# Kernel tuning notes

Hardware: AMD Instinct MI355X
Metric: run time of the kernel (lower is better)

The kernel has to match this reference:

```python
import jax, jax.numpy as jnp
import numpy as np

ROPE_BASE = 1000.0  # note: module uses base=1000, not the usual 10000


def _rope(x):
    # x: [B, L, H, d]; rotates the full head dim (x_pass is empty since d == hid_head)
    d = x.shape[-1]
    L = x.shape[1]
    theta = 1.0 / (ROPE_BASE ** (jnp.arange(0, d, 2, dtype=jnp.float32) / d))  # [d/2]
    idx = jnp.arange(L, dtype=jnp.float32)[:, None] * theta[None, :]            # [L, d/2]
    idx2 = jnp.concatenate([idx, idx], axis=-1)                                 # [L, d]
    cos = jnp.cos(idx2)[:, None, :]  # [L, 1, d] -> broadcasts over B, H
    sin = jnp.sin(idx2)[:, None, :]
    half = d // 2
    neg_half = jnp.concatenate([-x[..., half:], x[..., :half]], axis=-1)
    return x * cos + neg_half * sin


def setup_inputs() -> dict:
    key = jax.random.key(0)
    ks = jax.random.split(key, 8)
    B, Lq, Lc, F = 4, 1024, 2047, 2048
    s = 0.02
    return {
        "kv": jax.random.normal(ks[0], (B, 1, F), jnp.float32),
        "q": jax.random.normal(ks[1], (B, Lq, F), jnp.float32),
        "kv_cache": jax.random.normal(ks[2], (B, Lc, F, 2), jnp.float32),
        "Wq": jax.random.normal(ks[3], (F, F), jnp.float32) * s,
        "Wk": jax.random.normal(ks[4], (F, F), jnp.float32) * s,
        "Wv": jax.random.normal(ks[5], (F, F), jnp.float32) * s,
        "Wo": jax.random.normal(ks[6], (F, F), jnp.float32) * s,
        "mask": jnp.ones((B, 1, Lq, Lc + 1), jnp.int32),
        "num_heads": 16,
    }


def reference(kv, q, kv_cache, Wq, Wk, Wv, Wo, mask, num_heads):
    B = q.shape[0]
    F = Wq.shape[1]
    hd = F // num_heads

    query = q @ Wq                          # [B, Lq, F]
    key_new = kv[:, -1, :] @ Wk             # [B, F] (only last kv token is projected)
    val_new = kv[:, -1, :] @ Wv             # [B, F]

    key = jnp.concatenate([kv_cache[..., 0], key_new[:, None, :]], axis=1)    # [B, Lk, F]
    value = jnp.concatenate([kv_cache[..., 1], val_new[:, None, :]], axis=1)  # [B, Lk, F]
    kv_cache_out = jnp.stack([key, value], axis=-1)                            # [B, Lk, F, 2]

    query = query.reshape(B, -1, num_heads, hd)   # [B, Lq, H, d]
    key = key.reshape(B, -1, num_heads, hd)       # [B, Lk, H, d]
    value = value.reshape(B, -1, num_heads, hd)   # [B, Lk, H, d]

    query = _rope(query)
    key = _rope(key)

    aw = jnp.einsum('bqhd,bkhd->bhqk', query, key) / jnp.sqrt(jnp.float32(hd))
    aw = jnp.where(mask > 0, aw, -jnp.inf)  # mask [B,1,Lq,Lk] broadcasts over heads
    aw = jax.nn.softmax(aw, axis=-1)

    out = jnp.einsum('bhqk,bkhd->bqhd', aw, value).reshape(B, -1, F)
    logits = out @ Wo
    return logits, kv_cache_out
```

## Files before the change

### kernel.cpp

```cpp
#include <hip/hip_runtime.h>

#define B_  4
#define LQ  1024
#define LC  2047
#define LK  2048
#define F_  2048
#define H_  16
#define DH  128

typedef __attribute__((ext_vector_type(4))) float f32x4;
typedef __attribute__((ext_vector_type(8))) __bf16 bf16x8;
typedef __attribute__((ext_vector_type(8))) unsigned short u16x8;

#define GLD16(gp, lp)                                                          \
  __builtin_amdgcn_global_load_lds(                                            \
      (const __attribute__((address_space(1))) void*)(gp),                     \
      (__attribute__((address_space(3))) void*)(lp), 16, 0, 0)

__device__ __forceinline__ unsigned short f2bf(float f) {
  unsigned u = __float_as_uint(f);
  u += 0x7FFFu + ((u >> 16) & 1u);
  return (unsigned short)(u >> 16);
}
__device__ __forceinline__ unsigned short f2bf_trunc(float f) {
  return (unsigned short)(__float_as_uint(f) >> 16);
}
__device__ __forceinline__ float bf2f(unsigned short u) {
  return __uint_as_float((unsigned)u << 16);
}

__global__ void k_tables(float* __restrict__ cost, float* __restrict__ sint) {
  int pos = blockIdx.x, j = threadIdx.x;
  float theta = powf(1000.0f, -(float)j / 64.0f);
  float a = (float)pos * theta;
  cost[pos * 64 + j] = cosf(a);
  sint[pos * 64 + j] = sinf(a);
}

__global__ void k_gemv_part(const float* __restrict__ kv, const float* __restrict__ Wk,
                            const float* __restrict__ Wv, float* __restrict__ part) {
  __shared__ float kvs[4][256];
  int tid = threadIdx.x, z = blockIdx.z;
#pragma unroll
  for (int b = 0; b < 4; ++b) kvs[b][tid] = kv[b * F_ + z * 256 + tid];
  __syncthreads();
  const float* W = blockIdx.y ? Wv : Wk;
  int col = blockIdx.x * 256 + tid;
  float a0 = 0.f, a1 = 0.f, a2 = 0.f, a3 = 0.f;
  for (int k = 0; k < 256; ++k) {
    float w = W[(size_t)(z * 256 + k) * F_ + col];
    a0 = fmaf(kvs[0][k], w, a0);
    a1 = fmaf(kvs[1][k], w, a1);
    a2 = fmaf(kvs[2][k], w, a2);
    a3 = fmaf(kvs[3][k], w, a3);
  }
  float* o = part + (size_t)(blockIdx.y * 8 + z) * 8192;
  o[col] = a0; o[2048 + col] = a1; o[4096 + col] = a2; o[6144 + col] = a3;
}

__global__ void k_gemv_reduce(const float* __restrict__ part, float* __restrict__ knew,
                              float* __restrict__ vnew) {
  int t = blockIdx.x * 256 + threadIdx.x;
  int y = t >> 13, idx = t & 8191;
  float s = 0.f;
#pragma unroll
  for (int z = 0; z < 8; ++z) s += part[(size_t)(y * 8 + z) * 8192 + idx];
  (y ? vnew : knew)[idx] = s;
}

__global__ void k_prep_kv(const float* __restrict__ cache, const float* __restrict__ knew,
                          const float* __restrict__ vnew, const float* __restrict__ cost,
                          const float* __restrict__ sint, float* __restrict__ cache_out,
                          unsigned short* __restrict__ Kr, unsigned short* __restrict__ Vb) {
  int t = blockIdx.x * 256 + threadIdx.x;
  int j = t & 63, h = (t >> 6) & 15, pos = (t >> 10) & 2047, b = t >> 21;
  int f = h * DH + j;
  float k1, v1, k2, v2;
  if (pos < LC) {
    const float* p = cache + ((size_t)(b * LC + pos) * F_ + f) * 2;
    float2 x = *(const float2*)p;
    float2 y = *(const float2*)(p + 128);
    k1 = x.x; v1 = x.y; k2 = y.x; v2 = y.y;
  } else {
    k1 = knew[b * F_ + f];      v1 = vnew[b * F_ + f];
    k2 = knew[b * F_ + f + 64]; v2 = vnew[b * F_ + f + 64];
  }
  float* o = cache_out + ((size_t)(b * LK + pos) * F_ + f) * 2;
  *(float2*)o = make_float2(k1, v1);
  *(float2*)(o + 128) = make_float2(k2, v2);
  float c = cost[pos * 64 + j], s = sint[pos * 64 + j];
  size_t kb = ((size_t)(b * H_ + h) * LK + pos) * DH + j;
  Kr[kb]      = f2bf(k1 * c - k2 * s);
  Kr[kb + 64] = f2bf(k2 * c + k1 * s);
  Vb[kb]      = f2bf(v1);
  Vb[kb + 64] = f2bf(v2);
}

__global__ void k_transpose_w(const float* __restrict__ W, unsigned short* __restrict__ Wt) {
  __shared__ float tile[32][33];
  int n0 = blockIdx.x * 32, k0 = blockIdx.y * 32;
  int tx = threadIdx.x & 31, ty = threadIdx.x >> 5;
#pragma unroll
  for (int p = 0; p < 4; ++p)
    tile[ty + p * 8][tx] = W[(size_t)(k0 + ty + p * 8) * F_ + n0 + tx];
  __syncthreads();
#pragma unroll
  for (int p = 0; p < 4; ++p)
    Wt[(size_t)(n0 + ty + p * 8) * F_ + k0 + tx] = f2bf(tile[tx][ty + p * 8]);
}

__global__ void k_q_bf16(const float* __restrict__ x, unsigned short* __restrict__ y) {
  int t = blockIdx.x * 256 + threadIdx.x;
  float4 v = ((const float4*)x)[t];
  ushort4 o;
  o.x = f2bf(v.x); o.y = f2bf(v.y); o.z = f2bf(v.z); o.w = f2bf(v.w);
  ((ushort4*)y)[t] = o;
}

__global__ void k_rope_q(const unsigned short* __restrict__ qf, const float* __restrict__ cost,
                         const float* __restrict__ sint, unsigned short* __restrict__ Qro) {
  int t = blockIdx.x * 256 + threadIdx.x;
  int j = t & 63, h = (t >> 6) & 15, qi = (t >> 10) & 1023, b = t >> 20;
  const unsigned short* p = qf + ((size_t)(b * LQ + qi)) * F_ + h * DH + j;
  float a = bf2f(p[0]), a2 = bf2f(p[64]);
  float c = cost[qi * 64 + j], s = sint[qi * 64 + j];
  const float scale = 0.12751743343788055f;
  size_t ob = ((size_t)(b * H_ + h) * LQ + qi) * DH + j;
  Qro[ob]      = f2bf((a * c - a2 * s) * scale);
  Qro[ob + 64] = f2bf((a2 * c + a * s) * scale);
}

template <int BF16OUT>
__launch_bounds__(256)
__global__ void k_gemm(const unsigned short* __restrict__ A, const unsigned short* __restrict__ Bt,
                       void* __restrict__ Cv, int M, int N, int K) {
  __shared__ __align__(16) unsigned short As[128 * 32];
  __shared__ __align__(16) unsigned short Bs[128 * 32];
  int tid = threadIdx.x, wid = tid >> 6, l = tid & 63;
  int wm = wid >> 1, wn = wid & 1;
  int lr = l & 15, lg = l >> 4;
  int m0 = blockIdx.y * 128, n0 = blockIdx.x * 128;
  int row0 = tid >> 2, ch = tid & 3;
  const unsigned short* ga0 = A  + (size_t)(m0 + row0) * K + ch * 8;
  const unsigned short* ga1 = A  + (size_t)(m0 + row0 + 64) * K + ch * 8;
  const unsigned short* gb0 = Bt + (size_t)(n0 + row0) * K + ch * 8;
  const unsigned short* gb1 = Bt + (size_t)(n0 + row0 + 64) * K + ch * 8;
  f32x4 acc[4][4];
#pragma unroll
  for (int i = 0; i < 4; ++i)
#pragma unroll
    for (int j = 0; j < 4; ++j) acc[i][j] = (f32x4){0.f, 0.f, 0.f, 0.f};

  for (int kt = 0; kt < K; kt += 32) {
    __syncthreads();
    GLD16(ga0 + kt, As + tid * 8);
    GLD16(ga1 + kt, As + (tid + 256) * 8);
    GLD16(gb0 + kt, Bs + tid * 8);
    GLD16(gb1 + kt, Bs + (tid + 256) * 8);
    __syncthreads();
    bf16x8 af[4], bfr[4];
#pragma unroll
    for (int i = 0; i < 4; ++i) {
      af[i]  = *(const bf16x8*)&As[(wm * 64 + i * 16 + lr) * 32 + lg * 8];
      bfr[i] = *(const bf16x8*)&Bs[(wn * 64 + i * 16 + lr) * 32 + lg * 8];
    }
    __builtin_amdgcn_s_setprio(1);
#pragma unroll
    for (int mi = 0; mi < 4; ++mi)
#pragma unroll
      for (int ni = 0; ni < 4; ++ni)
        acc[mi][ni] = __builtin_amdgcn_mfma_f32_16x16x32_bf16(af[mi], bfr[ni], acc[mi][ni], 0, 0, 0);
    __builtin_amdgcn_s_setprio(0);
  }
#pragma unroll
  for (int mi = 0; mi < 4; ++mi)
#pragma unroll
    for (int ni = 0; ni < 4; ++ni) {
      int row = m0 + wm * 64 + mi * 16 + lg * 4;
      int col = n0 + wn * 64 + ni * 16 + lr;
#pragma unroll
      for (int r = 0; r < 4; ++r) {
        if (BF16OUT)
          ((unsigned short*)Cv)[(size_t)(row + r) * N + col] = f2bf(acc[mi][ni][r]);
        else
          ((float*)Cv)[(size_t)(row + r) * N + col] = acc[mi][ni][r];
      }
    }
}

__launch_bounds__(256, 2)
__global__ void k_attn(const unsigned short* __restrict__ Qr, const unsigned short* __restrict__ Kr,
                       const unsigned short* __restrict__ Vb, unsigned short* __restrict__ Oo) {
  __shared__ __align__(16) unsigned short Ks[64 * 128];
  __shared__ __align__(16) unsigned short Vt[128][72];
  __shared__ __align__(16) unsigned short Pb[4][32][72];
  int tid = threadIdx.x, wid = tid >> 6, l = tid & 63;
  int lr = l & 15, lg = l >> 4;
  int bh = blockIdx.x, q0 = blockIdx.y * 128 + wid * 32;
  const unsigned short* Qb = Qr + ((size_t)bh * LQ + q0) * DH;
  const unsigned short* Kb = Kr + (size_t)bh * LK * DH;
  const unsigned short* Vp = Vb + (size_t)bh * LK * DH;

  bf16x8 qf[2][4];
#pragma unroll
  for (int s = 0; s < 2; ++s)
#pragma unroll
    for (int c = 0; c < 4; ++c)
      qf[s][c] = *(const bf16x8*)(Qb + (size_t)(s * 16 + lr) * DH + c * 32 + lg * 8);

  const unsigned short* gk[4];
  unsigned short* lk[4];
#pragma unroll
  for (int p = 0; p < 4; ++p) {
    int g = tid + p * 256, row = g >> 4, cc = g & 15;
    gk[p] = Kb + (size_t)row * DH + (cc ^ (row & 7)) * 8;
    lk[p] = Ks + (size_t)g * 8;
  }

  f32x4 oacc[2][8];
#pragma unroll
  for (int s = 0; s < 2; ++s)
#pragma unroll
    for (int i = 0; i < 8; ++i) oacc[s][i] = (f32x4){0.f, 0.f, 0.f, 0.f};
  float mrun[2][4] = {{-1e30f, -1e30f, -1e30f, -1e30f}, {-1e30f, -1e30f, -1e30f, -1e30f}};
  float lpart[2][4] = {{0.f, 0.f, 0.f, 0.f}, {0.f, 0.f, 0.f, 0.f}};
  int sw = lr & 7;

  for (int kt = 0; kt < LK / 64; ++kt) {
    __syncthreads();
#pragma unroll
    for (int p = 0; p < 4; ++p) GLD16(gk[p] + (size_t)kt * 64 * DH, lk[p]);
    {
      int kp = tid >> 4, cg = tid & 15;
#pragma unroll
      for (int pp = 0; pp < 2; ++pp) {
        int kpp = kp + pp * 16;
        const unsigned short* src = Vp + (size_t)(kt * 64 + kpp * 2) * DH + cg * 8;
        u16x8 v0 = *(const u16x8*)(src);
        u16x8 v1 = *(const u16x8*)(src + DH);
        int kks = kpp ^ ((cg & 7) << 2);
#pragma unroll
        for (int e = 0; e < 8; ++e) {
          unsigned pack = (unsigned)v0[e] | ((unsigned)v1[e] << 16);
          *(unsigned*)&Vt[cg * 8 + e][kks * 2] = pack;
        }
      }
    }
    __syncthreads();

    f32x4 sf[2][4];
    __builtin_amdgcn_s_setprio(1);
#pragma unroll
    for (int ct = 0; ct < 4; ++ct) {
      f32x4 s0 = (f32x4){0.f, 0.f, 0.f, 0.f};
      f32x4 s1 = (f32x4){0.f, 0.f, 0.f, 0.f};
#pragma unroll
      for (int ck = 0; ck < 4; ++ck) {
        bf16x8 kf = *(const bf16x8*)&Ks[(ct * 16 + lr) * 128 + (((ck * 4 + lg) ^ sw) << 3)];
        s0 = __builtin_amdgcn_mfma_f32_16x16x32_bf16(qf[0][ck], kf, s0, 0, 0, 0);
        s1 = __builtin_amdgcn_mfma_f32_16x16x32_bf16(qf[1][ck], kf, s1, 0, 0, 0);
      }
      sf[0][ct] = s0; sf[1][ct] = s1;
    }
    __builtin_amdgcn_s_setprio(0);

    float pmax[2][4];
    bool allok = true;
#pragma unroll
    for (int s = 0; s < 2; ++s)
#pragma unroll
      for (int r = 0; r < 4; ++r) {
        pmax[s][r] = fmaxf(fmaxf(sf[s][0][r], sf[s][1][r]), fmaxf(sf[s][2][r], sf[s][3][r]));
        allok = allok && (pmax[s][r] - mrun[s][r] <= 8.0f);
      }
    if (!__all(allok)) {
#pragma unroll
      for (int s = 0; s < 2; ++s)
#pragma unroll
        for (int r = 0; r < 4; ++r) {
          float m = pmax[s][r];
#pragma unroll
          for (int off = 1; off < 16; off <<= 1) m = fmaxf(m, __shfl_xor(m, off));
          float mnew = fmaxf(mrun[s][r], m);
          float scl = exp2f(mrun[s][r] - mnew);
          lpart[s][r] *= scl;
#pragma unroll
          for (int dt = 0; dt < 8; ++dt) oacc[s][dt][r] *= scl;
          mrun[s][r] = mnew;
        }
    }
#pragma unroll
    for (int s = 0; s < 2; ++s)
#pragma unroll
      for (int r = 0; r < 4; ++r) {
#pragma unroll
        for (int ct = 0; ct < 4; ++ct) {
          float pe = exp2f(sf[s][ct][r] - mrun[s][r]);
          Pb[wid][s * 16 + lg * 4 + r][(ct * 16 + lr) ^ (lg << 3)] = f2bf_trunc(pe);
          lpart[s][r] += pe;
        }
      }

    int psw = (lg ^ (lr >> 2)) << 3;
    bf16x8 pf00 = *(const bf16x8*)&Pb[wid][lr][psw];
    bf16x8 pf01 = *(const bf16x8*)&Pb[wid][lr][32 + psw];
    bf16x8 pf10 = *(const bf16x8*)&Pb[wid][16 + lr][psw];
    bf16x8 pf11 = *(const bf16x8*)&Pb[wid][16 + lr][32 + psw];
    __builtin_amdgcn_s_setprio(1);
#pragma unroll
    for (int dt = 0; dt < 8; ++dt) {
      int d = dt * 16 + lr;
      int x = (d >> 3) & 7;
      bf16x8 v0 = *(const bf16x8*)&Vt[d][(lg ^ x) << 3];
      bf16x8 v1 = *(const bf16x8*)&Vt[d][((4 + lg) ^ x) << 3];
      oacc[0][dt] = __builtin_amdgcn_mfma_f32_16x16x32_bf16(pf00, v0, oacc[0][dt], 0, 0, 0);
      oacc[0][dt] = __builtin_amdgcn_mfma_f32_16x16x32_bf16(pf01, v1, oacc[0][dt], 0, 0, 0);
      oacc[1][dt] = __builtin_amdgcn_mfma_f32_16x16x32_bf16(pf10, v0, oacc[1][dt], 0, 0, 0);
      oacc[1][dt] = __builtin_amdgcn_mfma_f32_16x16x32_bf16(pf11, v1, oacc[1][dt], 0, 0, 0);
    }
    __builtin_amdgcn_s_setprio(0);
  }

  int b = bh >> 4, h = bh & 15;
#pragma unroll
  for (int s = 0; s < 2; ++s)
#pragma unroll
    for (int r = 0; r < 4; ++r) {
      float sum = lpart[s][r];
#pragma unroll
      for (int off = 1; off < 16; off <<= 1) sum += __shfl_xor(sum, off);
      float inv = 1.0f / sum;
      int qrow = q0 + s * 16 + lg * 4 + r;
      size_t base = ((size_t)(b * LQ + qrow)) * F_ + h * DH;
#pragma unroll
      for (int dt = 0; dt < 8; ++dt)
        Oo[base + dt * 16 + lr] = f2bf(oacc[s][dt][r] * inv);
    }
}

extern "C" void kernel_launch(void* const* d_in, const int* in_sizes, int n_in,
                              void* d_out, int out_size, void* d_ws, size_t ws_size,
                              hipStream_t stream) {
  const float* kv    = (const float*)d_in[0];
  const float* q     = (const float*)d_in[1];
  const float* cache = (const float*)d_in[2];
  const float* Wq    = (const float*)d_in[3];
  const float* Wk    = (const float*)d_in[4];
  const float* Wv    = (const float*)d_in[5];
  const float* Wo    = (const float*)d_in[6];

  float* logits    = (float*)d_out;
  float* cache_out = logits + (size_t)B_ * LQ * F_;

  char* ws = (char*)d_ws;
  float* cost          = (float*)(ws);
  float* sint          = (float*)(ws + 524288);
  float* knew          = (float*)(ws + 1048576);
  float* vnew          = (float*)(ws + 1081344);
  float* gpart         = (float*)(ws + 1114112);
  unsigned short* WqT  = (unsigned short*)(ws + 1638400);
  unsigned short* WoT  = (unsigned short*)(ws + 10027008);
  unsigned short* qbf  = (unsigned short*)(ws + 18415616);
  unsigned short* Qro  = (unsigned short*)(ws + 35192832);
  unsigned short* Kro  = (unsigned short*)(ws + 51970048);
  unsigned short* Vbf  = (unsigned short*)(ws + 85524480);
  unsigned short* qproj = (unsigned short*)(ws + 119078912);
  unsigned short* attno = (unsigned short*)(ws + 127467520);

  k_tables<<<dim3(LK), dim3(64), 0, stream>>>(cost, sint);
  k_gemv_part<<<dim3(8, 2, 8), dim3(256), 0, stream>>>(kv, Wk, Wv, gpart);
  k_gemv_reduce<<<dim3(64), dim3(256), 0, stream>>>(gpart, knew, vnew);
  k_prep_kv<<<dim3(32768), dim3(256), 0, stream>>>(cache, knew, vnew, cost, sint,
                                                   cache_out, Kro, Vbf);
  k_transpose_w<<<dim3(64, 64), dim3(256), 0, stream>>>(Wq, WqT);
  k_transpose_w<<<dim3(64, 64), dim3(256), 0, stream>>>(Wo, WoT);
  k_q_bf16<<<dim3(8192), dim3(256), 0, stream>>>(q, qbf);
  k_gemm<1><<<dim3(16, 32), dim3(256), 0, stream>>>(qbf, WqT, qproj, B_ * LQ, F_, F_);
  k_rope_q<<<dim3(16384), dim3(256), 0, stream>>>(qproj, cost, sint, Qro);
  k_attn<<<dim3(64, 8), dim3(256), 0, stream>>>(Qro, Kro, Vbf, attno);
  k_gemm<0><<<dim3(16, 32), dim3(256), 0, stream>>>(attno, WoT, logits, B_ * LQ, F_, F_);
}
```

Before: 333.9 us.

## Double-buffer K tiles and prefetch next tile during attention compute

The attention kernel now keeps two LDS buffers for K and issues async global-to-LDS loads for the next K tile before computing on the current one. V loads are issued at the top of each iteration so they overlap the barrier wait. The barriers are rebuilt with explicit waitcnt and s_barrier, so the Vt transpose write is fenced before the PV MFMA. The K swizzle widens from 8 to 16 chunks to cut LDS bank conflicts. LDS use grows by 16 KB per block, which may limit the two-blocks-per-CU occupancy, and the manual vmcnt counting is fragile.

```diff
diff --git a/kernel.cpp b/kernel.cpp
--- a/kernel.cpp
+++ b/kernel.cpp
@@ -7,6 +7,7 @@
 #define F_  2048
 #define H_  16
 #define DH  128
+#define NT  (LK / 64)
 
 typedef __attribute__((ext_vector_type(4))) float f32x4;
 typedef __attribute__((ext_vector_type(8))) __bf16 bf16x8;
@@ -191,7 +192,7 @@
 __launch_bounds__(256, 2)
 __global__ void k_attn(const unsigned short* __restrict__ Qr, const unsigned short* __restrict__ Kr,
                        const unsigned short* __restrict__ Vb, unsigned short* __restrict__ Oo) {
-  __shared__ __align__(16) unsigned short Ks[64 * 128];
+  __shared__ __align__(16) unsigned short KsB[2][64 * 128];
   __shared__ __align__(16) unsigned short Vt[128][72];
   __shared__ __align__(16) unsigned short Pb[4][32][72];
   int tid = threadIdx.x, wid = tid >> 6, l = tid & 63;
@@ -208,13 +209,12 @@
     for (int c = 0; c < 4; ++c)
       qf[s][c] = *(const bf16x8*)(Qb + (size_t)(s * 16 + lr) * DH + c * 32 + lg * 8);
 
-  const unsigned short* gk[4];
-  unsigned short* lk[4];
+  int gkoff[4], lkoff[4];
 #pragma unroll
   for (int p = 0; p < 4; ++p) {
     int g = tid + p * 256, row = g >> 4, cc = g & 15;
-    gk[p] = Kb + (size_t)row * DH + (cc ^ (row & 7)) * 8;
-    lk[p] = Ks + (size_t)g * 8;
+    gkoff[p] = row * DH + (cc ^ (row & 15)) * 8;
+    lkoff[p] = g * 8;
   }
 
   f32x4 oacc[2][8];
@@ -224,30 +224,42 @@
     for (int i = 0; i < 8; ++i) oacc[s][i] = (f32x4){0.f, 0.f, 0.f, 0.f};
   float mrun[2][4] = {{-1e30f, -1e30f, -1e30f, -1e30f}, {-1e30f, -1e30f, -1e30f, -1e30f}};
   float lpart[2][4] = {{0.f, 0.f, 0.f, 0.f}, {0.f, 0.f, 0.f, 0.f}};
-  int sw = lr & 7;
-
-  for (int kt = 0; kt < LK / 64; ++kt) {
-    __syncthreads();
-#pragma unroll
-    for (int p = 0; p < 4; ++p) GLD16(gk[p] + (size_t)kt * 64 * DH, lk[p]);
-    {
-      int kp = tid >> 4, cg = tid & 15;
-#pragma unroll
-      for (int pp = 0; pp < 2; ++pp) {
-        int kpp = kp + pp * 16;
-        const unsigned short* src = Vp + (size_t)(kt * 64 + kpp * 2) * DH + cg * 8;
-        u16x8 v0 = *(const u16x8*)(src);
-        u16x8 v1 = *(const u16x8*)(src + DH);
-        int kks = kpp ^ ((cg & 7) << 2);
-#pragma unroll
-        for (int e = 0; e < 8; ++e) {
-          unsigned pack = (unsigned)v0[e] | ((unsigned)v1[e] << 16);
-          *(unsigned*)&Vt[cg * 8 + e][kks * 2] = pack;
-        }
-      }
-    }
-    __syncthreads();
-
+
+#pragma unroll
+  for (int p = 0; p < 4; ++p) GLD16(Kb + gkoff[p], &KsB[0][lkoff[p]]);
+
+  int kp = tid >> 4, cg = tid & 15;
+  const unsigned short* vsrc = Vp + (size_t)(kp * 2) * DH + cg * 8;
+
+  for (int kt = 0; kt < NT; ++kt) {
+    int cur = kt & 1;
+    u16x8 v00 = *(const u16x8*)(vsrc);
+    u16x8 v01 = *(const u16x8*)(vsrc + DH);
+    u16x8 v10 = *(const u16x8*)(vsrc + 32 * DH);
+    u16x8 v11 = *(const u16x8*)(vsrc + 33 * DH);
+    vsrc += 64 * DH;
+    __builtin_amdgcn_sched_barrier(0);
+    const unsigned short* Kn = Kb + (size_t)((kt + 1 < NT) ? (kt + 1) * 64 * DH : 0);
+#pragma unroll
+    for (int p = 0; p < 4; ++p) GLD16(Kn + gkoff[p], &KsB[cur ^ 1][lkoff[p]]);
+    asm volatile("s_waitcnt vmcnt(4)" ::: "memory");
+    __builtin_amdgcn_sched_barrier(0);
+    __builtin_amdgcn_s_barrier();
+    __builtin_amdgcn_sched_barrier(0);
+
+#pragma unroll
+    for (int pp = 0; pp < 2; ++pp) {
+      int kpp = kp + pp * 16;
+      int kks = kpp ^ ((cg & 7) << 2);
+      u16x8 a = pp ? v10 : v00, b2 = pp ? v11 : v01;
+#pragma unroll
+      for (int e = 0; e < 8; ++e) {
+        unsigned pack = (unsigned)a[e] | ((unsigned)b2[e] << 16);
+        *(unsigned*)&Vt[cg * 8 + e][kks * 2] = pack;
+      }
+    }
+
+    const unsigned short* Kcur = KsB[cur];
     f32x4 sf[2][4];
     __builtin_amdgcn_s_setprio(1);
 #pragma unroll
@@ -256,7 +268,7 @@
       f32x4 s1 = (f32x4){0.f, 0.f, 0.f, 0.f};
 #pragma unroll
       for (int ck = 0; ck < 4; ++ck) {
-        bf16x8 kf = *(const bf16x8*)&Ks[(ct * 16 + lr) * 128 + (((ck * 4 + lg) ^ sw) << 3)];
+        bf16x8 kf = *(const bf16x8*)&Kcur[(ct * 16 + lr) * 128 + (((ck * 4 + lg) ^ lr) << 3)];
         s0 = __builtin_amdgcn_mfma_f32_16x16x32_bf16(qf[0][ck], kf, s0, 0, 0, 0);
         s1 = __builtin_amdgcn_mfma_f32_16x16x32_bf16(qf[1][ck], kf, s1, 0, 0, 0);
       }
@@ -300,6 +312,11 @@
           lpart[s][r] += pe;
         }
       }
+
+    asm volatile("s_waitcnt lgkmcnt(0)" ::: "memory");
+    __builtin_amdgcn_sched_barrier(0);
+    __builtin_amdgcn_s_barrier();
+    __builtin_amdgcn_sched_barrier(0);
 
     int psw = (lg ^ (lr >> 2)) << 3;
     bf16x8 pf00 = *(const bf16x8*)&Pb[wid][lr][psw];
```

Result: no change. 328.6 us (-1.6%).

## Split attention key range across two warp halves and swizzle GEMM block order

Applied to the files above, without the earlier changes.

The attention kernel now runs 512 threads per block. Two groups of four waves each process half of the key sequence for the same query rows, using 32-key tiles, and their partial softmax states and outputs are merged through shared memory at the end. The V tile loads are software-prefetched one iteration ahead in registers with explicit waitcnt control, and the K swizzle is widened. The GEMM also remaps block indices with a swizzle for better L2 locality. This raises per-CU parallelism and overlap, at the cost of smaller tiles per sync, an extra merge step with a bf16 rounding of the partial output, and higher register and LDS pressure.

```diff
diff --git a/kernel.cpp b/kernel.cpp
--- a/kernel.cpp
+++ b/kernel.cpp
@@ -139,7 +139,10 @@
   int tid = threadIdx.x, wid = tid >> 6, l = tid & 63;
   int wm = wid >> 1, wn = wid & 1;
   int lr = l & 15, lg = l >> 4;
-  int m0 = blockIdx.y * 128, n0 = blockIdx.x * 128;
+  int nwg = gridDim.x * gridDim.y;
+  int lin = blockIdx.y * gridDim.x + blockIdx.x;
+  int swz = (lin & 7) * (nwg >> 3) + (lin >> 3);
+  int m0 = (swz / gridDim.x) * 128, n0 = (swz % gridDim.x) * 128;
   int row0 = tid >> 2, ch = tid & 3;
   const unsigned short* ga0 = A  + (size_t)(m0 + row0) * K + ch * 8;
   const unsigned short* ga1 = A  + (size_t)(m0 + row0 + 64) * K + ch * 8;
@@ -188,18 +191,25 @@
     }
 }
 
-__launch_bounds__(256, 2)
+__launch_bounds__(512, 4)
 __global__ void k_attn(const unsigned short* __restrict__ Qr, const unsigned short* __restrict__ Kr,
                        const unsigned short* __restrict__ Vb, unsigned short* __restrict__ Oo) {
-  __shared__ __align__(16) unsigned short Ks[64 * 128];
-  __shared__ __align__(16) unsigned short Vt[128][72];
-  __shared__ __align__(16) unsigned short Pb[4][32][72];
+  __shared__ __align__(16) unsigned char SM[57344];
+  unsigned short* KS = (unsigned short*)SM;
+  unsigned short* VT = (unsigned short*)(SM + 16384);
+  unsigned short* PB = (unsigned short*)(SM + 36864);
+
   int tid = threadIdx.x, wid = tid >> 6, l = tid & 63;
   int lr = l & 15, lg = l >> 4;
-  int bh = blockIdx.x, q0 = blockIdx.y * 128 + wid * 32;
+  int half = wid >> 2, wq = wid & 3, lt = tid & 255;
+  int bh = blockIdx.x, q0 = blockIdx.y * 128 + wq * 32;
   const unsigned short* Qb = Qr + ((size_t)bh * LQ + q0) * DH;
-  const unsigned short* Kb = Kr + (size_t)bh * LK * DH;
-  const unsigned short* Vp = Vb + (size_t)bh * LK * DH;
+  const unsigned short* Kb = Kr + ((size_t)bh * LK + half * 1024) * DH;
+  const unsigned short* Vp = Vb + ((size_t)bh * LK + half * 1024) * DH;
+
+  unsigned short* KSh = KS + half * (32 * 128);
+  unsigned short* VTh = VT + half * (128 * 40);
+  unsigned short* PBw = PB + wid * (32 * 40);
 
   bf16x8 qf[2][4];
 #pragma unroll
@@ -208,14 +218,15 @@
     for (int c = 0; c < 4; ++c)
       qf[s][c] = *(const bf16x8*)(Qb + (size_t)(s * 16 + lr) * DH + c * 32 + lg * 8);
 
-  const unsigned short* gk[4];
-  unsigned short* lk[4];
-#pragma unroll
-  for (int p = 0; p < 4; ++p) {
-    int g = tid + p * 256, row = g >> 4, cc = g & 15;
-    gk[p] = Kb + (size_t)row * DH + (cc ^ (row & 7)) * 8;
-    lk[p] = Ks + (size_t)g * 8;
-  }
+  int gko[2], lko[2];
+#pragma unroll
+  for (int p = 0; p < 2; ++p) {
+    int g = lt + p * 256, row = g >> 4, cc = g & 15;
+    gko[p] = row * DH + ((cc ^ (row & 15)) * 8);
+    lko[p] = g * 8;
+  }
+  int kp = lt >> 4, cg = lt & 15;
+  int kks = (kp ^ ((cg & 3) << 2)) * 2;
 
   f32x4 oacc[2][8];
 #pragma unroll
@@ -224,39 +235,41 @@
     for (int i = 0; i < 8; ++i) oacc[s][i] = (f32x4){0.f, 0.f, 0.f, 0.f};
   float mrun[2][4] = {{-1e30f, -1e30f, -1e30f, -1e30f}, {-1e30f, -1e30f, -1e30f, -1e30f}};
   float lpart[2][4] = {{0.f, 0.f, 0.f, 0.f}, {0.f, 0.f, 0.f, 0.f}};
-  int sw = lr & 7;
-
-  for (int kt = 0; kt < LK / 64; ++kt) {
+
+  const unsigned short* vs0 = Vp + (size_t)(kp * 2) * DH + cg * 8;
+  u16x8 v0 = *(const u16x8*)vs0;
+  u16x8 v1 = *(const u16x8*)(vs0 + DH);
+
+  for (int t = 0; t < 32; ++t) {
     __syncthreads();
-#pragma unroll
-    for (int p = 0; p < 4; ++p) GLD16(gk[p] + (size_t)kt * 64 * DH, lk[p]);
+    GLD16(Kb + (size_t)t * 32 * DH + gko[0], KSh + lko[0]);
+    GLD16(Kb + (size_t)t * 32 * DH + gko[1], KSh + lko[1]);
+    asm volatile("s_waitcnt vmcnt(2)" ::: "memory");
+    __builtin_amdgcn_sched_barrier(0);
+#pragma unroll
+    for (int e = 0; e < 8; ++e) {
+      unsigned pk = (unsigned)v0[e] | ((unsigned)v1[e] << 16);
+      *(unsigned*)&VTh[(cg * 8 + e) * 40 + kks] = pk;
+    }
     {
-      int kp = tid >> 4, cg = tid & 15;
-#pragma unroll
-      for (int pp = 0; pp < 2; ++pp) {
-        int kpp = kp + pp * 16;
-        const unsigned short* src = Vp + (size_t)(kt * 64 + kpp * 2) * DH + cg * 8;
-        u16x8 v0 = *(const u16x8*)(src);
-        u16x8 v1 = *(const u16x8*)(src + DH);
-        int kks = kpp ^ ((cg & 7) << 2);
-#pragma unroll
-        for (int e = 0; e < 8; ++e) {
-          unsigned pack = (unsigned)v0[e] | ((unsigned)v1[e] << 16);
-          *(unsigned*)&Vt[cg * 8 + e][kks * 2] = pack;
-        }
-      }
-    }
+      int tn = (t + 1 < 32) ? t + 1 : t;
+      const unsigned short* vn = Vp + (size_t)(tn * 32 + kp * 2) * DH + cg * 8;
+      v0 = *(const u16x8*)vn;
+      v1 = *(const u16x8*)(vn + DH);
+    }
+    asm volatile("s_waitcnt vmcnt(2) lgkmcnt(0)" ::: "memory");
+    __builtin_amdgcn_sched_barrier(0);
     __syncthreads();
 
-    f32x4 sf[2][4];
+    f32x4 sf[2][2];
     __builtin_amdgcn_s_setprio(1);
 #pragma unroll
-    for (int ct = 0; ct < 4; ++ct) {
+    for (int ct = 0; ct < 2; ++ct) {
       f32x4 s0 = (f32x4){0.f, 0.f, 0.f, 0.f};
       f32x4 s1 = (f32x4){0.f, 0.f, 0.f, 0.f};
 #pragma unroll
       for (int ck = 0; ck < 4; ++ck) {
-        bf16x8 kf = *(const bf16x8*)&Ks[(ct * 16 + lr) * 128 + (((ck * 4 + lg) ^ sw) << 3)];
+        bf16x8 kf = *(const bf16x8*)&KSh[(ct * 16 + lr) * 128 + (((ck * 4 + lg) ^ lr) << 3)];
         s0 = __builtin_amdgcn_mfma_f32_16x16x32_bf16(qf[0][ck], kf, s0, 0, 0, 0);
         s1 = __builtin_amdgcn_mfma_f32_16x16x32_bf16(qf[1][ck], kf, s1, 0, 0, 0);
       }
@@ -270,7 +283,7 @@
     for (int s = 0; s < 2; ++s)
 #pragma unroll
       for (int r = 0; r < 4; ++r) {
-        pmax[s][r] = fmaxf(fmaxf(sf[s][0][r], sf[s][1][r]), fmaxf(sf[s][2][r], sf[s][3][r]));
+        pmax[s][r] = fmaxf(sf[s][0][r], sf[s][1][r]);
         allok = allok && (pmax[s][r] - mrun[s][r] <= 8.0f);
       }
     if (!__all(allok)) {
@@ -294,48 +307,76 @@
 #pragma unroll
       for (int r = 0; r < 4; ++r) {
 #pragma unroll
-        for (int ct = 0; ct < 4; ++ct) {
+        for (int ct = 0; ct < 2; ++ct) {
           float pe = exp2f(sf[s][ct][r] - mrun[s][r]);
-          Pb[wid][s * 16 + lg * 4 + r][(ct * 16 + lr) ^ (lg << 3)] = f2bf_trunc(pe);
+          PBw[(s * 16 + lg * 4 + r) * 40 + ((ct * 16 + lr) ^ (lg << 3))] = f2bf_trunc(pe);
           lpart[s][r] += pe;
         }
       }
+    asm volatile("s_waitcnt lgkmcnt(0)" ::: "memory");
+    __builtin_amdgcn_sched_barrier(0);
 
     int psw = (lg ^ (lr >> 2)) << 3;
-    bf16x8 pf00 = *(const bf16x8*)&Pb[wid][lr][psw];
-    bf16x8 pf01 = *(const bf16x8*)&Pb[wid][lr][32 + psw];
-    bf16x8 pf10 = *(const bf16x8*)&Pb[wid][16 + lr][psw];
-    bf16x8 pf11 = *(const bf16x8*)&Pb[wid][16 + lr][32 + psw];
+    bf16x8 pf0 = *(const bf16x8*)&PBw[lr * 40 + psw];
+    bf16x8 pf1 = *(const bf16x8*)&PBw[(16 + lr) * 40 + psw];
     __builtin_amdgcn_s_setprio(1);
 #pragma unroll
     for (int dt = 0; dt < 8; ++dt) {
       int d = dt * 16 + lr;
-      int x = (d >> 3) & 7;
-      bf16x8 v0 = *(const bf16x8*)&Vt[d][(lg ^ x) << 3];
-      bf16x8 v1 = *(const bf16x8*)&Vt[d][((4 + lg) ^ x) << 3];
-      oacc[0][dt] = __builtin_amdgcn_mfma_f32_16x16x32_bf16(pf00, v0, oacc[0][dt], 0, 0, 0);
-      oacc[0][dt] = __builtin_amdgcn_mfma_f32_16x16x32_bf16(pf01, v1, oacc[0][dt], 0, 0, 0);
-      oacc[1][dt] = __builtin_amdgcn_mfma_f32_16x16x32_bf16(pf10, v0, oacc[1][dt], 0, 0, 0);
-      oacc[1][dt] = __builtin_amdgcn_mfma_f32_16x16x32_bf16(pf11, v1, oacc[1][dt], 0, 0, 0);
+      int x = (d >> 3) & 3;
+      bf16x8 v = *(const bf16x8*)&VTh[d * 40 + ((lg ^ x) << 3)];
+      oacc[0][dt] = __builtin_amdgcn_mfma_f32_16x16x32_bf16(pf0, v, oacc[0][dt], 0, 0, 0);
+      oacc[1][dt] = __builtin_amdgcn_mfma_f32_16x16x32_bf16(pf1, v, oacc[1][dt], 0, 0, 0);
     }
     __builtin_amdgcn_s_setprio(0);
   }
 
-  int b = bh >> 4, h = bh & 15;
+  float lsum[2][4];
 #pragma unroll
   for (int s = 0; s < 2; ++s)
 #pragma unroll
     for (int r = 0; r < 4; ++r) {
-      float sum = lpart[s][r];
-#pragma unroll
-      for (int off = 1; off < 16; off <<= 1) sum += __shfl_xor(sum, off);
-      float inv = 1.0f / sum;
-      int qrow = q0 + s * 16 + lg * 4 + r;
-      size_t base = ((size_t)(b * LQ + qrow)) * F_ + h * DH;
-#pragma unroll
-      for (int dt = 0; dt < 8; ++dt)
-        Oo[base + dt * 16 + lr] = f2bf(oacc[s][dt][r] * inv);
-    }
+      float t2 = lpart[s][r];
+#pragma unroll
+      for (int off = 1; off < 16; off <<= 1) t2 += __shfl_xor(t2, off);
+      lsum[s][r] = t2;
+    }
+  __syncthreads();
+  unsigned short* OHI = (unsigned short*)SM;
+  float2* ML = (float2*)(SM + 32768);
+
+  if (half == 1) {
+#pragma unroll
+    for (int s = 0; s < 2; ++s)
+#pragma unroll
+      for (int r = 0; r < 4; ++r) {
+        int q = s * 16 + lg * 4 + r;
+#pragma unroll
+        for (int dt = 0; dt < 8; ++dt)
+          OHI[(wq * 32 + q) * 128 + dt * 16 + lr] = f2bf(oacc[s][dt][r]);
+        if (lr == 0) ML[wq * 32 + q] = make_float2(mrun[s][r], lsum[s][r]);
+      }
+  }
+  __syncthreads();
+  if (half == 0) {
+    int b = bh >> 4, h = bh & 15;
+#pragma unroll
+    for (int s = 0; s < 2; ++s)
+#pragma unroll
+      for (int r = 0; r < 4; ++r) {
+        int q = s * 16 + lg * 4 + r;
+        float2 ml = ML[wq * 32 + q];
+        float M = fmaxf(mrun[s][r], ml.x);
+        float e0 = exp2f(mrun[s][r] - M), e1 = exp2f(ml.x - M);
+        float inv = 1.0f / (lsum[s][r] * e0 + ml.y * e1);
+        size_t base = ((size_t)(b * LQ + q0 + q)) * F_ + h * DH;
+#pragma unroll
+        for (int dt = 0; dt < 8; ++dt) {
+          float hi = bf2f(OHI[(wq * 32 + q) * 128 + dt * 16 + lr]);
+          Oo[base + dt * 16 + lr] = f2bf((oacc[s][dt][r] * e0 + hi * e1) * inv);
+        }
+      }
+  }
 }
 
 extern "C" void kernel_launch(void* const* d_in, const int* in_sizes, int n_in,
@@ -377,6 +418,6 @@
   k_q_bf16<<<dim3(8192), dim3(256), 0, stream>>>(q, qbf);
   k_gemm<1><<<dim3(16, 32), dim3(256), 0, stream>>>(qbf, WqT, qproj, B_ * LQ, F_, F_);
   k_rope_q<<<dim3(16384), dim3(256), 0, stream>>>(qproj, cost, sint, Qro);
-  k_attn<<<dim3(64, 8), dim3(256), 0, stream>>>(Qro, Kro, Vbf, attno);
+  k_attn<<<dim3(64, 8), dim3(512), 0, stream>>>(Qro, Kro, Vbf, attno);
   k_gemm<0><<<dim3(16, 32), dim3(256), 0, stream>>>(attno, WoT, logits, B_ * LQ, F_, F_);
 }
```

New measurement: 826.5 us (median of 2 runs). 2.48x slower.
